# Kernel tuning notes

Hardware: AMD Instinct MI355X
Metric: run time of the kernel (lower is better)

Reference implementation:

```python
import jax, jax.numpy as jnp
import numpy as np

N, C_TOTAL, C, H, W = 8, 448, 100, 56, 56


def setup_inputs() -> dict:
    key = jax.random.key(0)
    k1, k2, k3, k4 = jax.random.split(key, 4)
    fmaps = jax.random.normal(k1, (N, C_TOTAL, H, W), dtype=jnp.float32)
    select_index = jax.random.randint(k2, (C,), 0, C_TOTAL)
    mean = jax.random.normal(k3, (C, H, W), dtype=jnp.float32)
    # Per-pixel inverse covariance must be PSD so the quadratic form is >= 0
    A = jax.random.normal(k4, (C, C, H, W), dtype=jnp.float32)
    cov = jnp.einsum('cehw,dehw->cdhw', A, A) / jnp.float32(C)  # (C,C,H,W), PSD per pixel
    return {
        'fmaps': fmaps,
        'select_index': select_index,
        'mean': mean,
        'cov': cov,
        'min_score': jnp.float32(0.0),
        'max_score': jnp.float32(50.0),
    }


def reference(fmaps, select_index, mean, cov, min_score, max_score):
    # x_ = fmaps[:, select_index, ...] - mean  -> (N, C, H, W)
    x = fmaps[:, select_index, :, :] - mean[None]
    # left = sum_c x[n,c,h,w] * cov[c,d,h,w]  (per-pixel matvec), avoids (N,C,C,H,W) intermediate
    left = jnp.einsum('nchw,cdhw->ndhw', x, cov)
    # per-pixel Mahalanobis distance
    s_map = jnp.sqrt(jnp.sum(x * left, axis=1))  # (N, H, W)
    # bilinear upsample x4 (torch Upsample align_corners=False == half-pixel linear resize)
    score_map = jax.image.resize(s_map, (s_map.shape[0], 4 * H, 4 * W), method='linear')
    scores = (score_map - min_score) / (max_score - min_score)
    return jnp.squeeze(scores)
```

## Files before the change

### kernel.cpp

```cpp
#include <hip/hip_runtime.h>
#include <math.h>

#define NN 8
#define C_TOTAL 448
#define CC 100
#define HH 56
#define WW 56
#define HW (HH*WW)
#define NPIX4 (HW/4)
#define OH 224
#define OW 224
#define NPAIR 50
#define NT4 13

typedef __attribute__((ext_vector_type(4))) _Float16 half4;

__device__ __forceinline__ void fma4(float4& acc, const float4 a, const float4 b) {
    acc.x = fmaf(a.x, b.x, acc.x);
    acc.y = fmaf(a.y, b.y, acc.y);
    acc.z = fmaf(a.z, b.z, acc.z);
    acc.w = fmaf(a.w, b.w, acc.w);
}
__device__ __forceinline__ float4 h2f(const half4 h) {
    float4 r; r.x = (float)h.x; r.y = (float)h.y; r.z = (float)h.z; r.w = (float)h.w;
    return r;
}

__global__ __launch_bounds__(256) void prep_x_kernel(
    const float* __restrict__ fmaps, const int* __restrict__ sel,
    const float* __restrict__ mean, half4* __restrict__ xbuf)
{
    const int idx = blockIdx.x * 256 + threadIdx.x;
    const int total = NN * CC * NPIX4;
    if (idx >= total) return;
    const int p4 = idx % NPIX4;
    const int c  = (idx / NPIX4) % CC;
    const int n  = idx / (NPIX4 * CC);

    const float4* f4 = (const float4*)fmaps;
    const float4* m4 = (const float4*)mean;

    const float4 f = f4[((size_t)n * C_TOTAL + sel[c]) * NPIX4 + p4];
    const float4 m = m4[(size_t)c * NPIX4 + p4];
    half4 r;
    r.x = (_Float16)(f.x - m.x);
    r.y = (_Float16)(f.y - m.y);
    r.z = (_Float16)(f.z - m.z);
    r.w = (_Float16)(f.w - m.w);
    xbuf[((size_t)n * CC + c) * NPIX4 + p4] = r;
}

__global__ __launch_bounds__(512) void qform_kernel(
    const half4* __restrict__ xbuf, const float* __restrict__ cov,
    float* __restrict__ qpart)
{
    const int tile = blockIdx.x % NT4;
    const int r    = blockIdx.x / NT4;
    const int s    = 99 - r;
    const int n    = threadIdx.x >> 6;
    const int p4   = tile * 64 + (threadIdx.x & 63);
    if (p4 >= NPIX4) return;

    const half4*  x4 = xbuf + (size_t)n * CC * NPIX4;
    const float4* c4 = (const float4*)cov;

    const float4* covr = c4 + ((size_t)r * CC + r) * NPIX4 + p4;
    const float4* covs = c4 + ((size_t)s * CC + s) * NPIX4 + p4;
    const half4*  xp   = x4 + (size_t)r * NPIX4 + p4;

    float4 ir = make_float4(0.f, 0.f, 0.f, 0.f);
    float4 is = make_float4(0.f, 0.f, 0.f, 0.f);

    const float4 xr = h2f(*xp);
    {
        float4 h; h.x = 0.5f*xr.x; h.y = 0.5f*xr.y; h.z = 0.5f*xr.z; h.w = 0.5f*xr.w;
        fma4(ir, h, *covr);
    }
    xp += NPIX4; covr += NPIX4;

    int d = r + 1;
    for (; d + 3 < s; d += 4) {
        const half4  h0 = xp[0], h1 = xp[NPIX4], h2 = xp[2*NPIX4], h3 = xp[3*NPIX4];
        const float4 g0 = covr[0], g1 = covr[NPIX4], g2 = covr[2*NPIX4], g3 = covr[3*NPIX4];
        fma4(ir, h2f(h0), g0);
        fma4(ir, h2f(h1), g1);
        fma4(ir, h2f(h2), g2);
        fma4(ir, h2f(h3), g3);
        xp += 4*NPIX4; covr += 4*NPIX4;
    }
    for (; d < s; ++d) {
        fma4(ir, h2f(*xp), *covr);
        xp += NPIX4; covr += NPIX4;
    }

    const float4 xs = h2f(*xp);
    fma4(ir, xs, *covr);
    {
        float4 h; h.x = 0.5f*xs.x; h.y = 0.5f*xs.y; h.z = 0.5f*xs.z; h.w = 0.5f*xs.w;
        fma4(is, h, *covs);
    }
    xp += NPIX4; covr += NPIX4; covs += NPIX4;

    d = s + 1;
    for (; d + 3 < CC; d += 4) {
        const half4  h0 = xp[0], h1 = xp[NPIX4], h2 = xp[2*NPIX4], h3 = xp[3*NPIX4];
        const float4 a0 = covr[0], a1 = covr[NPIX4], a2 = covr[2*NPIX4], a3 = covr[3*NPIX4];
        const float4 b0 = covs[0], b1 = covs[NPIX4], b2 = covs[2*NPIX4], b3 = covs[3*NPIX4];
        const float4 f0 = h2f(h0), f1 = h2f(h1), f2 = h2f(h2), f3 = h2f(h3);
        fma4(ir, f0, a0); fma4(is, f0, b0);
        fma4(ir, f1, a1); fma4(is, f1, b1);
        fma4(ir, f2, a2); fma4(is, f2, b2);
        fma4(ir, f3, a3); fma4(is, f3, b3);
        xp += 4*NPIX4; covr += 4*NPIX4; covs += 4*NPIX4;
    }
    for (; d < CC; ++d) {
        const float4 f0 = h2f(*xp);
        fma4(ir, f0, *covr);
        fma4(is, f0, *covs);
        xp += NPIX4; covr += NPIX4; covs += NPIX4;
    }

    float4 q;
    q.x = 2.0f * (fmaf(xr.x, ir.x, xs.x * is.x));
    q.y = 2.0f * (fmaf(xr.y, ir.y, xs.y * is.y));
    q.z = 2.0f * (fmaf(xr.z, ir.z, xs.z * is.z));
    q.w = 2.0f * (fmaf(xr.w, ir.w, xs.w * is.w));

    float4* qp = (float4*)qpart;
    qp[((size_t)r * NN + n) * NPIX4 + p4] = q;
}

__global__ __launch_bounds__(256) void reduce_kernel(
    const float* __restrict__ qpart, float* __restrict__ smap)
{
    const int idx = blockIdx.x * 256 + threadIdx.x;
    if (idx >= NN * NPIX4) return;
    const int p4 = idx % NPIX4;
    const int n  = idx / NPIX4;

    const float4* qp = (const float4*)qpart;
    float4 acc = make_float4(0.f, 0.f, 0.f, 0.f);
#pragma unroll
    for (int k = 0; k < NPAIR; ++k) {
        const float4 v = qp[((size_t)k * NN + n) * NPIX4 + p4];
        acc.x += v.x; acc.y += v.y; acc.z += v.z; acc.w += v.w;
    }
    float4 o;
    o.x = sqrtf(fmaxf(acc.x, 0.f));
    o.y = sqrtf(fmaxf(acc.y, 0.f));
    o.z = sqrtf(fmaxf(acc.z, 0.f));
    o.w = sqrtf(fmaxf(acc.w, 0.f));
    ((float4*)smap)[(size_t)n * NPIX4 + p4] = o;
}

__global__ __launch_bounds__(256) void upsample_kernel(
    const float* __restrict__ smap,
    const float* __restrict__ minp, const float* __restrict__ maxp,
    float* __restrict__ out)
{
    const int idx = blockIdx.x * 256 + threadIdx.x;
    const int total = NN * OH * OW;
    if (idx >= total) return;

    const int ox = idx % OW;
    const int oy = (idx / OW) % OH;
    const int n  = idx / (OW * OH);

    const float fy = oy * 0.25f - 0.375f;
    const float fx = ox * 0.25f - 0.375f;

    int y0 = (int)floorf(fy);
    int x0 = (int)floorf(fx);
    const float wy = fy - (float)y0;
    const float wx = fx - (float)x0;
    int y1 = min(y0 + 1, HH - 1); y0 = max(y0, 0);
    int x1 = min(x0 + 1, WW - 1); x0 = max(x0, 0);

    const float* s = smap + (size_t)n * HW;
    const float v00 = s[y0 * WW + x0];
    const float v01 = s[y0 * WW + x1];
    const float v10 = s[y1 * WW + x0];
    const float v11 = s[y1 * WW + x1];

    const float v = (1.0f - wy) * ((1.0f - wx) * v00 + wx * v01)
                  +          wy * ((1.0f - wx) * v10 + wx * v11);

    const float mn = *minp;
    const float mx = *maxp;
    out[idx] = (v - mn) / (mx - mn);
}

extern "C" void kernel_launch(void* const* d_in, const int* in_sizes, int n_in,
                              void* d_out, int out_size, void* d_ws, size_t ws_size,
                              hipStream_t stream)
{
    const float* fmaps = (const float*)d_in[0];
    const int*   sel   = (const int*)  d_in[1];
    const float* mean  = (const float*)d_in[2];
    const float* cov   = (const float*)d_in[3];
    const float* minp  = (const float*)d_in[4];
    const float* maxp  = (const float*)d_in[5];
    float* out = (float*)d_out;

    half4* xbuf  = (half4*)d_ws;
    float* qpart = (float*)((char*)d_ws + (size_t)NN*CC*HW*2);
    float* smap  = qpart + (size_t)NPAIR * NN * HW;

    {
        const int total = NN * CC * NPIX4;
        prep_x_kernel<<<(total + 255) / 256, 256, 0, stream>>>(fmaps, sel, mean, xbuf);
    }
    qform_kernel<<<NT4 * NPAIR, 512, 0, stream>>>(xbuf, cov, qpart);
    {
        const int total = NN * NPIX4;
        reduce_kernel<<<(total + 255) / 256, 256, 0, stream>>>(qpart, smap);
    }
    {
        const int total = NN * OH * OW;
        upsample_kernel<<<(total + 255) / 256, 256, 0, stream>>>(smap, minp, maxp, out);
    }
}
```

Before: 235.5 us.

## Give each row its own block and reduce with atomics into score map

Replaces the paired-row scheme (row r with row 99-r, 50 blocks per tile) with one block per row r, giving 100 row-blocks per tile that each accumulate the upper-triangle product. Per-row partial quadratic forms are added into a zeroed score map with float atomics, which removes the 50-way partial buffer and the separate reduce kernel. The sqrt moves into the upsample kernel. Per-block work is now imbalanced across rows, and the atomic accumulation order is nondeterministic. The sqrt is also recomputed four times per output pixel.

```diff
diff --git a/kernel.cpp b/kernel.cpp
--- a/kernel.cpp
+++ b/kernel.cpp
@@ -10,7 +10,6 @@
 #define NPIX4 (HW/4)
 #define OH 224
 #define OW 224
-#define NPAIR 50
 #define NT4 13
 
 typedef __attribute__((ext_vector_type(4))) _Float16 half4;
@@ -50,13 +49,18 @@
     xbuf[((size_t)n * CC + c) * NPIX4 + p4] = r;
 }
 
+__global__ __launch_bounds__(256) void zero_kernel(float4* __restrict__ smap2)
+{
+    const int idx = blockIdx.x * 256 + threadIdx.x;
+    if (idx < NN * NPIX4) smap2[idx] = make_float4(0.f, 0.f, 0.f, 0.f);
+}
+
 __global__ __launch_bounds__(512) void qform_kernel(
     const half4* __restrict__ xbuf, const float* __restrict__ cov,
-    float* __restrict__ qpart)
+    float* __restrict__ smap2)
 {
     const int tile = blockIdx.x % NT4;
     const int r    = blockIdx.x / NT4;
-    const int s    = 99 - r;
     const int n    = threadIdx.x >> 6;
     const int p4   = tile * 64 + (threadIdx.x & 63);
     if (p4 >= NPIX4) return;
@@ -64,97 +68,44 @@
     const half4*  x4 = xbuf + (size_t)n * CC * NPIX4;
     const float4* c4 = (const float4*)cov;
 
-    const float4* covr = c4 + ((size_t)r * CC + r) * NPIX4 + p4;
-    const float4* covs = c4 + ((size_t)s * CC + s) * NPIX4 + p4;
+    const float4* covp = c4 + ((size_t)r * CC + r) * NPIX4 + p4;
     const half4*  xp   = x4 + (size_t)r * NPIX4 + p4;
 
-    float4 ir = make_float4(0.f, 0.f, 0.f, 0.f);
-    float4 is = make_float4(0.f, 0.f, 0.f, 0.f);
-
     const float4 xr = h2f(*xp);
+    float4 acc;
     {
-        float4 h; h.x = 0.5f*xr.x; h.y = 0.5f*xr.y; h.z = 0.5f*xr.z; h.w = 0.5f*xr.w;
-        fma4(ir, h, *covr);
+        const float4 cd = *covp;
+        acc.x = 0.5f * xr.x * cd.x;
+        acc.y = 0.5f * xr.y * cd.y;
+        acc.z = 0.5f * xr.z * cd.z;
+        acc.w = 0.5f * xr.w * cd.w;
     }
-    xp += NPIX4; covr += NPIX4;
+    xp += NPIX4; covp += NPIX4;
 
     int d = r + 1;
-    for (; d + 3 < s; d += 4) {
+    for (; d + 3 < CC; d += 4) {
         const half4  h0 = xp[0], h1 = xp[NPIX4], h2 = xp[2*NPIX4], h3 = xp[3*NPIX4];
-        const float4 g0 = covr[0], g1 = covr[NPIX4], g2 = covr[2*NPIX4], g3 = covr[3*NPIX4];
-        fma4(ir, h2f(h0), g0);
-        fma4(ir, h2f(h1), g1);
-        fma4(ir, h2f(h2), g2);
-        fma4(ir, h2f(h3), g3);
-        xp += 4*NPIX4; covr += 4*NPIX4;
+        const float4 g0 = covp[0], g1 = covp[NPIX4], g2 = covp[2*NPIX4], g3 = covp[3*NPIX4];
+        fma4(acc, h2f(h0), g0);
+        fma4(acc, h2f(h1), g1);
+        fma4(acc, h2f(h2), g2);
+        fma4(acc, h2f(h3), g3);
+        xp += 4*NPIX4; covp += 4*NPIX4;
     }
-    for (; d < s; ++d) {
-        fma4(ir, h2f(*xp), *covr);
-        xp += NPIX4; covr += NPIX4;
+    for (; d < CC; ++d) {
+        fma4(acc, h2f(*xp), *covp);
+        xp += NPIX4; covp += NPIX4;
     }
 
-    const float4 xs = h2f(*xp);
-    fma4(ir, xs, *covr);
-    {
-        float4 h; h.x = 0.5f*xs.x; h.y = 0.5f*xs.y; h.z = 0.5f*xs.z; h.w = 0.5f*xs.w;
-        fma4(is, h, *covs);
-    }
-    xp += NPIX4; covr += NPIX4; covs += NPIX4;
-
-    d = s + 1;
-    for (; d + 3 < CC; d += 4) {
-        const half4  h0 = xp[0], h1 = xp[NPIX4], h2 = xp[2*NPIX4], h3 = xp[3*NPIX4];
-        const float4 a0 = covr[0], a1 = covr[NPIX4], a2 = covr[2*NPIX4], a3 = covr[3*NPIX4];
-        const float4 b0 = covs[0], b1 = covs[NPIX4], b2 = covs[2*NPIX4], b3 = covs[3*NPIX4];
-        const float4 f0 = h2f(h0), f1 = h2f(h1), f2 = h2f(h2), f3 = h2f(h3);
-        fma4(ir, f0, a0); fma4(is, f0, b0);
-        fma4(ir, f1, a1); fma4(is, f1, b1);
-        fma4(ir, f2, a2); fma4(is, f2, b2);
-        fma4(ir, f3, a3); fma4(is, f3, b3);
-        xp += 4*NPIX4; covr += 4*NPIX4; covs += 4*NPIX4;
-    }
-    for (; d < CC; ++d) {
-        const float4 f0 = h2f(*xp);
-        fma4(ir, f0, *covr);
-        fma4(is, f0, *covs);
-        xp += NPIX4; covr += NPIX4; covs += NPIX4;
-    }
-
-    float4 q;
-    q.x = 2.0f * (fmaf(xr.x, ir.x, xs.x * is.x));
-    q.y = 2.0f * (fmaf(xr.y, ir.y, xs.y * is.y));
-    q.z = 2.0f * (fmaf(xr.z, ir.z, xs.z * is.z));
-    q.w = 2.0f * (fmaf(xr.w, ir.w, xs.w * is.w));
-
-    float4* qp = (float4*)qpart;
-    qp[((size_t)r * NN + n) * NPIX4 + p4] = q;
-}
-
-__global__ __launch_bounds__(256) void reduce_kernel(
-    const float* __restrict__ qpart, float* __restrict__ smap)
-{
-    const int idx = blockIdx.x * 256 + threadIdx.x;
-    if (idx >= NN * NPIX4) return;
-    const int p4 = idx % NPIX4;
-    const int n  = idx / NPIX4;
-
-    const float4* qp = (const float4*)qpart;
-    float4 acc = make_float4(0.f, 0.f, 0.f, 0.f);
-#pragma unroll
-    for (int k = 0; k < NPAIR; ++k) {
-        const float4 v = qp[((size_t)k * NN + n) * NPIX4 + p4];
-        acc.x += v.x; acc.y += v.y; acc.z += v.z; acc.w += v.w;
-    }
-    float4 o;
-    o.x = sqrtf(fmaxf(acc.x, 0.f));
-    o.y = sqrtf(fmaxf(acc.y, 0.f));
-    o.z = sqrtf(fmaxf(acc.z, 0.f));
-    o.w = sqrtf(fmaxf(acc.w, 0.f));
-    ((float4*)smap)[(size_t)n * NPIX4 + p4] = o;
+    float* sp = smap2 + (size_t)n * HW + 4 * p4;
+    unsafeAtomicAdd(sp + 0, 2.0f * xr.x * acc.x);
+    unsafeAtomicAdd(sp + 1, 2.0f * xr.y * acc.y);
+    unsafeAtomicAdd(sp + 2, 2.0f * xr.z * acc.z);
+    unsafeAtomicAdd(sp + 3, 2.0f * xr.w * acc.w);
 }
 
 __global__ __launch_bounds__(256) void upsample_kernel(
-    const float* __restrict__ smap,
+    const float* __restrict__ smap2,
     const float* __restrict__ minp, const float* __restrict__ maxp,
     float* __restrict__ out)
 {
@@ -176,11 +127,11 @@
     int y1 = min(y0 + 1, HH - 1); y0 = max(y0, 0);
     int x1 = min(x0 + 1, WW - 1); x0 = max(x0, 0);
 
-    const float* s = smap + (size_t)n * HW;
-    const float v00 = s[y0 * WW + x0];
-    const float v01 = s[y0 * WW + x1];
-    const float v10 = s[y1 * WW + x0];
-    const float v11 = s[y1 * WW + x1];
+    const float* s = smap2 + (size_t)n * HW;
+    const float v00 = sqrtf(fmaxf(s[y0 * WW + x0], 0.f));
+    const float v01 = sqrtf(fmaxf(s[y0 * WW + x1], 0.f));
+    const float v10 = sqrtf(fmaxf(s[y1 * WW + x0], 0.f));
+    const float v11 = sqrtf(fmaxf(s[y1 * WW + x1], 0.f));
 
     const float v = (1.0f - wy) * ((1.0f - wx) * v00 + wx * v01)
                   +          wy * ((1.0f - wx) * v10 + wx * v11);
@@ -203,20 +154,19 @@
     float* out = (float*)d_out;
 
     half4* xbuf  = (half4*)d_ws;
-    float* qpart = (float*)((char*)d_ws + (size_t)NN*CC*HW*2);
-    float* smap  = qpart + (size_t)NPAIR * NN * HW;
+    float* smap2 = (float*)((char*)d_ws + (size_t)NN*CC*HW*2);
 
     {
         const int total = NN * CC * NPIX4;
         prep_x_kernel<<<(total + 255) / 256, 256, 0, stream>>>(fmaps, sel, mean, xbuf);
     }
-    qform_kernel<<<NT4 * NPAIR, 512, 0, stream>>>(xbuf, cov, qpart);
     {
         const int total = NN * NPIX4;
-        reduce_kernel<<<(total + 255) / 256, 256, 0, stream>>>(qpart, smap);
+        zero_kernel<<<(total + 255) / 256, 256, 0, stream>>>((float4*)smap2);
     }
+    qform_kernel<<<NT4 * CC, 512, 0, stream>>>(xbuf, cov, smap2);
     {
         const int total = NN * OH * OW;
-        upsample_kernel<<<(total + 255) / 256, 256, 0, stream>>>(smap, minp, maxp, out);
+        upsample_kernel<<<(total + 255) / 256, 256, 0, stream>>>(smap2, minp, maxp, out);
     }
 }
```

After: 250.8 us. 1.07x slower.

## Share cov rows across batch waves via double-buffered async global-to-LDS loads

Applied to the files above, without the earlier changes.

The quadratic-form kernel previously had each of the 8 batch waves read the same cov row elements from global memory on its own. It now has the 8 waves cooperatively stage 8 cov entries per chunk into LDS with global_load_lds, double-buffered, and every wave reads all of them from shared memory. This cuts redundant global and L2 traffic for cov by up to 8x. In exchange it adds two block barriers per chunk, per-element branching on the r/s split, and one padded extra row load, while x is still read from global.

```diff
diff --git a/kernel.cpp b/kernel.cpp
--- a/kernel.cpp
+++ b/kernel.cpp
@@ -12,6 +12,7 @@
 #define OW 224
 #define NPAIR 50
 #define NT4 13
+#define NCHUNK 13
 
 typedef __attribute__((ext_vector_type(4))) _Float16 half4;
 
@@ -24,6 +25,12 @@
 __device__ __forceinline__ float4 h2f(const half4 h) {
     float4 r; r.x = (float)h.x; r.y = (float)h.y; r.z = (float)h.z; r.w = (float)h.w;
     return r;
+}
+
+__device__ __forceinline__ void gload16(const void* g, void* l) {
+    __builtin_amdgcn_global_load_lds(
+        (const __attribute__((address_space(1))) unsigned int*)g,
+        (__attribute__((address_space(3))) unsigned int*)l, 16, 0, 0);
 }
 
 __global__ __launch_bounds__(256) void prep_x_kernel(
@@ -54,80 +61,67 @@
     const half4* __restrict__ xbuf, const float* __restrict__ cov,
     float* __restrict__ qpart)
 {
+    __shared__ float4 sbuf[2][8][64];
+
     const int tile = blockIdx.x % NT4;
     const int r    = blockIdx.x / NT4;
-    const int s    = 99 - r;
-    const int n    = threadIdx.x >> 6;
-    const int p4   = tile * 64 + (threadIdx.x & 63);
-    if (p4 >= NPIX4) return;
-
-    const half4*  x4 = xbuf + (size_t)n * CC * NPIX4;
-    const float4* c4 = (const float4*)cov;
-
-    const float4* covr = c4 + ((size_t)r * CC + r) * NPIX4 + p4;
-    const float4* covs = c4 + ((size_t)s * CC + s) * NPIX4 + p4;
-    const half4*  xp   = x4 + (size_t)r * NPIX4 + p4;
-
-    float4 ir = make_float4(0.f, 0.f, 0.f, 0.f);
-    float4 is = make_float4(0.f, 0.f, 0.f, 0.f);
-
-    const float4 xr = h2f(*xp);
-    {
-        float4 h; h.x = 0.5f*xr.x; h.y = 0.5f*xr.y; h.z = 0.5f*xr.z; h.w = 0.5f*xr.w;
-        fma4(ir, h, *covr);
-    }
-    xp += NPIX4; covr += NPIX4;
-
-    int d = r + 1;
-    for (; d + 3 < s; d += 4) {
-        const half4  h0 = xp[0], h1 = xp[NPIX4], h2 = xp[2*NPIX4], h3 = xp[3*NPIX4];
-        const float4 g0 = covr[0], g1 = covr[NPIX4], g2 = covr[2*NPIX4], g3 = covr[3*NPIX4];
-        fma4(ir, h2f(h0), g0);
-        fma4(ir, h2f(h1), g1);
-        fma4(ir, h2f(h2), g2);
-        fma4(ir, h2f(h3), g3);
-        xp += 4*NPIX4; covr += 4*NPIX4;
-    }
-    for (; d < s; ++d) {
-        fma4(ir, h2f(*xp), *covr);
-        xp += NPIX4; covr += NPIX4;
-    }
-
-    const float4 xs = h2f(*xp);
-    fma4(ir, xs, *covr);
-    {
-        float4 h; h.x = 0.5f*xs.x; h.y = 0.5f*xs.y; h.z = 0.5f*xs.z; h.w = 0.5f*xs.w;
-        fma4(is, h, *covs);
-    }
-    xp += NPIX4; covr += NPIX4; covs += NPIX4;
-
-    d = s + 1;
-    for (; d + 3 < CC; d += 4) {
-        const half4  h0 = xp[0], h1 = xp[NPIX4], h2 = xp[2*NPIX4], h3 = xp[3*NPIX4];
-        const float4 a0 = covr[0], a1 = covr[NPIX4], a2 = covr[2*NPIX4], a3 = covr[3*NPIX4];
-        const float4 b0 = covs[0], b1 = covs[NPIX4], b2 = covs[2*NPIX4], b3 = covs[3*NPIX4];
-        const float4 f0 = h2f(h0), f1 = h2f(h1), f2 = h2f(h2), f3 = h2f(h3);
-        fma4(ir, f0, a0); fma4(is, f0, b0);
-        fma4(ir, f1, a1); fma4(is, f1, b1);
-        fma4(ir, f2, a2); fma4(is, f2, b2);
-        fma4(ir, f3, a3); fma4(is, f3, b3);
-        xp += 4*NPIX4; covr += 4*NPIX4; covs += 4*NPIX4;
-    }
-    for (; d < CC; ++d) {
-        const float4 f0 = h2f(*xp);
-        fma4(ir, f0, *covr);
-        fma4(is, f0, *covs);
-        xp += NPIX4; covr += NPIX4; covs += NPIX4;
-    }
-
-    float4 q;
-    q.x = 2.0f * (fmaf(xr.x, ir.x, xs.x * is.x));
-    q.y = 2.0f * (fmaf(xr.y, ir.y, xs.y * is.y));
-    q.z = 2.0f * (fmaf(xr.z, ir.z, xs.z * is.z));
-    q.w = 2.0f * (fmaf(xr.w, ir.w, xs.w * is.w));
-
-    float4* qp = (float4*)qpart;
-    qp[((size_t)r * NN + n) * NPIX4 + p4] = q;
+    const int s    = CC - 1 - r;
+    const int w    = threadIdx.x >> 6;
+    const int lane = threadIdx.x & 63;
+    const int qraw = tile * 64 + lane;
+    const bool valid = qraw < NPIX4;
+    const int quad = valid ? qraw : (NPIX4 - 1);
+
+    const int splitc = 100 - r;
+
+    auto stage = [&](int k, int b) {
+        int c = k * 8 + w;
+        if (c > 100) c = 100;
+        const bool inR = (c < splitc);
+        const int row = inR ? r : s;
+        const int d   = inR ? (r + c) : (s + (c - splitc));
+        const float4* src = (const float4*)cov + ((size_t)row * CC + d) * NPIX4 + quad;
+        gload16((const void*)src, (void*)&sbuf[b][w][lane]);
+    };
+
+    const half4* xn = xbuf + (size_t)w * CC * NPIX4;
+
+    float4 accR = make_float4(0.f, 0.f, 0.f, 0.f);
+    float4 accS = make_float4(0.f, 0.f, 0.f, 0.f);
+
+    stage(0, 0);
+    for (int k = 0; k < NCHUNK; ++k) {
+        if (k + 1 < NCHUNK) stage(k + 1, (k + 1) & 1);
+        __syncthreads();
+
+        const int b = k & 1;
+#pragma unroll
+        for (int j = 0; j < 8; ++j) {
+            const int c = k * 8 + j;
+            if (c > 100) break;
+            const bool inR = (c < splitc);
+            const int d = inR ? (r + c) : (s + (c - splitc));
+            const float wgt = (c == 0 || c == splitc) ? 0.5f : 1.0f;
+
+            const float4 cv = sbuf[b][j][lane];
+            float4 xd = h2f(xn[(size_t)d * NPIX4 + quad]);
+            xd.x *= wgt; xd.y *= wgt; xd.z *= wgt; xd.w *= wgt;
+            if (inR) fma4(accR, xd, cv);
+            else     fma4(accS, xd, cv);
+        }
+        __syncthreads();
+    }
+
+    if (valid) {
+        const float4 xr = h2f(xn[(size_t)r * NPIX4 + quad]);
+        const float4 xs = h2f(xn[(size_t)s * NPIX4 + quad]);
+        float4 q;
+        q.x = 2.0f * fmaf(xr.x, accR.x, xs.x * accS.x);
+        q.y = 2.0f * fmaf(xr.y, accR.y, xs.y * accS.y);
+        q.z = 2.0f * fmaf(xr.z, accR.z, xs.z * accS.z);
+        q.w = 2.0f * fmaf(xr.w, accR.w, xs.w * accS.w);
+        ((float4*)qpart)[((size_t)r * NN + w) * NPIX4 + qraw] = q;
+    }
 }
 
 __global__ __launch_bounds__(256) void reduce_kernel(
@@ -176,11 +170,11 @@
     int y1 = min(y0 + 1, HH - 1); y0 = max(y0, 0);
     int x1 = min(x0 + 1, WW - 1); x0 = max(x0, 0);
 
-    const float* s = smap + (size_t)n * HW;
-    const float v00 = s[y0 * WW + x0];
-    const float v01 = s[y0 * WW + x1];
-    const float v10 = s[y1 * WW + x0];
-    const float v11 = s[y1 * WW + x1];
+    const float* sm = smap + (size_t)n * HW;
+    const float v00 = sm[y0 * WW + x0];
+    const float v01 = sm[y0 * WW + x1];
+    const float v10 = sm[y1 * WW + x0];
+    const float v11 = sm[y1 * WW + x1];
 
     const float v = (1.0f - wy) * ((1.0f - wx) * v00 + wx * v01)
                   +          wy * ((1.0f - wx) * v10 + wx * v11);
@@ -203,7 +197,7 @@
     float* out = (float*)d_out;
 
     half4* xbuf  = (half4*)d_ws;
-    float* qpart = (float*)((char*)d_ws + (size_t)NN*CC*HW*2);
+    float* qpart = (float*)((char*)d_ws + (size_t)NN*CC*NPIX4*8);
     float* smap  = qpart + (size_t)NPAIR * NN * HW;
 
     {
```

Result: no change. 239.9 us (+1.9%).
